# Optimization experiments

Measured on AMD Instinct MI355X. Metric: run time of the kernel, lower is better.

Reference implementation:

```python
import jax, jax.numpy as jnp
import numpy as np

ALPHA = 0.01
EPSB = ALPHA / (1.0 - 2.0 * ALPHA)  # boundary_eps
BIG = 1e9  # stands in for +inf; all real boundary distances are << box diameter


def setup_inputs() -> dict:
    key = jax.random.key(0)
    ks = jax.random.split(key, 8)
    B, D, K = 32768, 16, 1024
    return {
        "x": jax.random.normal(ks[0], (B, D), jnp.float32),
        "logp": jnp.zeros((B, 1), jnp.float32),
        "an1_w": 0.1 * jax.random.normal(ks[1], (D,), jnp.float32),
        "an1_b": 0.1 * jax.random.normal(ks[2], (D,), jnp.float32),
        "an2_w": 0.1 * jax.random.normal(ks[3], (D,), jnp.float32),
        "an2_b": 0.1 * jax.random.normal(ks[4], (D,), jnp.float32),
        "shift_coeff": jax.random.normal(ks[5], (D,), jnp.float32),
        "anchor_raw": jax.random.normal(ks[6], (1, K, D), jnp.float32),  # vorproj._anchor_pts
        "box_min": -4.0 * jnp.ones((D,), jnp.float32),
        "box_max": 4.0 * jnp.ones((D,), jnp.float32),
        "mixture_logits": jnp.zeros((K,), jnp.float32),
    }


def reference(x, logp, an1_w, an1_b, an2_w, an2_b, shift_coeff,
              anchor_raw, box_min, box_max, mixture_logits):
    B, D = x.shape
    # --- actnorm1: y = (x + b) * exp(w); logdet = sum(w) ---
    x = (x + an1_b) * jnp.exp(an1_w)
    logp = logp - jnp.sum(an1_w)
    # --- logit_transform.inverse: y = (sigmoid(x) - alpha) / (1 - 2*alpha) ---
    ld = jnp.sum(jax.nn.log_sigmoid(x) + jax.nn.log_sigmoid(-x), axis=1, keepdims=True) \
         - D * jnp.log(1.0 - 2.0 * ALPHA)
    x = (jax.nn.sigmoid(x) - ALPHA) / (1.0 - 2.0 * ALPHA)
    logp = logp - ld
    # --- (-eps, 1+eps) -> (0, 1) ---
    span = 1.0 + 2.0 * EPSB
    x = (x + EPSB) / span
    logp = logp + D * jnp.log(span)
    # --- scale into box constraints ---
    scale = box_max - box_min  # (D,)
    x = x * scale + box_min
    logp = logp - jnp.sum(jnp.log(scale))
    # --- anchor points: R -> (-1,1) -> (0,1) -> box ---
    a = anchor_raw[0]                       # (K, D)
    a = a / (1.0 + jnp.abs(a))
    a = (a + 1.0) * 0.5 * scale + box_min   # (K, D)
    K = a.shape[0]
    # --- find_nearest: argmin_k ||x - a_k||^2 (drop const ||x||^2) ---
    a_sq = jnp.sum(a * a, axis=1)                    # (K,)
    d2 = a_sq[None, :] - 2.0 * (x @ a.T)             # (B, K)
    k = jnp.argmin(d2, axis=1)                       # (B,)
    mask = jax.nn.one_hot(k, K, dtype=bool).reshape(B, 1, K)
    x_k = a[k]                                       # (B, D) gathered anchor
    # --- shift toward anchor: x + c*(x_k - x); logdet = sum log(1-c) ---
    c = jax.nn.sigmoid(shift_coeff) * 0.98 + 0.01
    x = x + c * (x_k - x)
    logp = logp - jnp.sum(jnp.log1p(-c))
    # --- map_outside_cell: radial map of Voronoi cell (within box) onto R^D ---
    dx = x - x_k
    r = jnp.sqrt(jnp.sum(dx * dx, axis=1))           # (B,)
    u = dx / jnp.maximum(r, 1e-12)[:, None]          # (B, D) unit direction
    # half-plane boundary distance t_j = (||a_j - a_k||^2 / 2) / (u . (a_j - a_k))
    proj = u @ a.T - jnp.sum(u * x_k, axis=1, keepdims=True)              # (B, K)
    halfdist = 0.5 * (a_sq[None, :] + a_sq[k][:, None] - 2.0 * (x_k @ a.T))  # (B, K)
    self_mask = jnp.arange(K)[None, :] == k[:, None]
    valid = jnp.logical_and(jnp.logical_not(self_mask), proj > 1e-12)
    t_half = jnp.where(valid, halfdist / jnp.where(valid, proj, 1.0), BIG)
    # box-face distances along u
    up = u > 1e-12
    un = u < -1e-12
    t_box = jnp.where(up, (box_max[None, :] - x_k) / jnp.where(up, u, 1.0),
            jnp.where(un, (box_min[None, :] - x_k) / jnp.where(un, u, 1.0), BIG))
    t = jnp.minimum(jnp.min(t_half, axis=1), jnp.min(t_box, axis=1))      # (B,)
    ratio = r / t                                     # in [0, 0.99] after shift
    s = 1.0 / (1.0 - ratio)
    x = x_k + dx * s[:, None]
    # logdet = (D+1) * log(t / (t - r)) = -(D+1) * log1p(-ratio)
    logp = logp + (D + 1.0) * jnp.log1p(-ratio)[:, None]
    # --- subtract cell center ---
    x = x - x_k
    # --- actnorm2 ---
    x = (x + an2_b) * jnp.exp(an2_w)
    logp = logp - jnp.sum(an2_w)
    # --- mixture component log-prob ---
    logprobs = jax.nn.log_softmax(mixture_logits)
    logp = logp - logprobs[k][:, None]
    return x, logp, mask
```

## Files before the change

kernel.cpp:

```cpp
#include <hip/hip_runtime.h>
#include <math.h>

#define DD 16
#define KK 1024

#define WS_A    0
#define WS_ASQ  16384
#define WS_OMC  17408
#define WS_B2   17424
#define WS_E2   17440
#define WS_MN   17456
#define WS_MX   17472
#define WS_SCL  17488
#define WS_DIM  17504
#define WS_E1   17520
#define WS_BASE 17536
#define WS_TOTD 17537
#define WS_NEED_BYTES (WS_TOTD * 8)

__device__ __forceinline__ double xformD(double rv, double mn, double scl) {
  double t = rv / (1.0 + fabs(rv));
  return (t + 1.0) * 0.5 * scl + mn;
}
__device__ __forceinline__ float xformF(float v, float mn, float mx) {
  return (v / (1.f + fabsf(v)) + 1.f) * 0.5f * (mx - mn) + mn;
}

__global__ __launch_bounds__(256) void vor_pre(
    const float* __restrict__ an1_w, const float* __restrict__ an2_w,
    const float* __restrict__ an2_b, const float* __restrict__ shift_c,
    const float* __restrict__ anchor_raw,
    const float* __restrict__ box_min, const float* __restrict__ box_max,
    const float* __restrict__ mlogits, double* __restrict__ ws)
{
  __shared__ double redD[16];
  const int tid = threadIdx.x;
  const int blk = blockIdx.x;

  if (blk == 0 && tid < DD) {
    double w1 = (double)an1_w[tid], w2 = (double)an2_w[tid];
    double sgc = 1.0 / (1.0 + exp(-(double)shift_c[tid]));
    double c = sgc * 0.98 + 0.01;
    double mn = (double)box_min[tid], mx = (double)box_max[tid];
    ws[WS_OMC + tid] = 1.0 - c;
    ws[WS_B2  + tid] = (double)an2_b[tid];
    ws[WS_E2  + tid] = exp(w2);
    ws[WS_MN  + tid] = mn;
    ws[WS_MX  + tid] = mx;
    ws[WS_SCL + tid] = mx - mn;
    ws[WS_E1  + tid] = exp(w1);
    ws[WS_DIM + tid] = -w1 - log(mx - mn) - log1p(-c) - w2;
  }
  const int j0 = blk * 64;
  for (int e = tid; e < 64 * DD; e += 256) {
    int j = j0 + (e >> 4), d = e & 15;
    double mn = (double)box_min[d];
    double scl = (double)box_max[d] - mn;
    ws[WS_A + (size_t)j * DD + d] = xformD((double)anchor_raw[j * DD + d], mn, scl);
  }
  __syncthreads();
  for (int j = j0 + tid; j < j0 + 64; j += 256) {
    double s = 0.0;
    #pragma unroll
    for (int d = 0; d < DD; ++d) { double a = ws[WS_A + (size_t)j * DD + d]; s = fma(a, a, s); }
    ws[WS_ASQ + j] = s;
  }
  if (blk != 0) return;
  float lm = -3.4e38f;
  for (int i = tid; i < KK; i += 256) lm = fmaxf(lm, mlogits[i]);
  #pragma unroll
  for (int o = 32; o > 0; o >>= 1) lm = fmaxf(lm, __shfl_xor(lm, o));
  if ((tid & 63) == 0) redD[tid >> 6] = (double)lm;
  __syncthreads();
  float gmax = (float)fmax(fmax(redD[0], redD[1]), fmax(redD[2], redD[3]));
  double lsum = 0.0;
  for (int i = tid; i < KK; i += 256) lsum += exp((double)mlogits[i] - (double)gmax);
  #pragma unroll
  for (int o = 32; o > 0; o >>= 1) lsum += __shfl_xor(lsum, o);
  if ((tid & 63) == 0) redD[4 + (tid >> 6)] = lsum;
  __syncthreads();
  if (tid == 0) {
    double lse = (double)gmax + log(redD[4] + redD[5] + redD[6] + redD[7]);
    double b = (double)DD * (log(0.98) + log(1.0 + 2.0 * (0.01 / 0.98)));
    #pragma unroll
    for (int d = 0; d < DD; ++d) b += ws[WS_DIM + d];
    ws[WS_BASE] = b + lse;
  }
}

#define NT2 1024
#define RPB2 128
#define SL2 8
#define JSL2 (KK / SL2)

__global__ __launch_bounds__(NT2, 4) void vor2(
    const float* __restrict__ x_in, const float* __restrict__ logp_in,
    const float* __restrict__ an1_b,
    const float* __restrict__ mlogits, const double* __restrict__ ws,
    float* __restrict__ out, int Brows)
{
  __shared__ __align__(16) float sA[KK][DD];
  __shared__ float sAsqH[KK];
  __shared__ float sX4T[DD][RPB2];
  __shared__ int   sPj[16][64];
  __shared__ float sRat[16][64];
  __shared__ int   sK[RPB2];
  __shared__ float sOmcF[DD], sB2F[DD], sE2F[DD], sMnF[DD], sMxF[DD];

  const int tid  = threadIdx.x;
  const int w    = tid >> 6;
  const int lane = tid & 63;
  const int rg   = w >> 3;
  const int sl   = w & 7;
  const int rrow = rg * 64 + lane;
  const int row  = blockIdx.x * RPB2 + rrow;
  const size_t coreEnd = (size_t)Brows * (DD + 1);

  if (tid < DD) {
    sOmcF[tid] = (float)ws[WS_OMC + tid];
    sB2F[tid]  = (float)ws[WS_B2 + tid];
    sE2F[tid]  = (float)ws[WS_E2 + tid];
    sMnF[tid]  = (float)ws[WS_MN + tid];
    sMxF[tid]  = (float)ws[WS_MX + tid];
  }
  for (int e = tid; e < KK * DD / 4; e += NT2) {
    double2 p0 = ((const double2*)(ws + WS_A))[e * 2 + 0];
    double2 p1 = ((const double2*)(ws + WS_A))[e * 2 + 1];
    ((float4*)sA)[e] = make_float4((float)p0.x, (float)p0.y, (float)p1.x, (float)p1.y);
  }
  __syncthreads();
  for (int j = tid; j < KK; j += NT2) {
    float acc = 0.f;
    #pragma unroll
    for (int d = 0; d < DD; ++d) { float a = sA[j][d]; acc = fmaf(a, a, acc); }
    sAsqH[j] = 0.5f * acc;
  }
  {
    float4* mz = (float4*)(out + coreEnd + (size_t)blockIdx.x * RPB2 * KK);
    #pragma unroll 4
    for (int i = tid; i < RPB2 * KK / 4; i += NT2)
      mz[i] = make_float4(0.f, 0.f, 0.f, 0.f);
  }

  const double A = 0.01, EPSB = 0.01 / 0.98;
  const double SPAN = 1.0 + 2.0 * EPSB;
  double lsigD = 0.0;
  if (sl == 0) {
    const float* xr = x_in + (size_t)row * DD;
    #pragma unroll
    for (int d = 0; d < DD; ++d) {
      double y1 = ((double)xr[d] + (double)an1_b[d]) * ws[WS_E1 + d];
      double sg = 1.0 / (1.0 + exp(-y1));
      double x2 = (sg - A) / (1.0 - 2.0 * A);
      double x3 = (x2 + EPSB) / SPAN;
      double x4 = x3 * ws[WS_SCL + d] + ws[WS_MN + d];
      sX4T[d][rrow] = (float)x4;
      double ay = fabs(y1);
      lsigD += ay + 2.0 * log1p(exp(-ay));
    }
  }
  __syncthreads();

  float x4f[DD];
  #pragma unroll
  for (int d = 0; d < DD; ++d) x4f[d] = sX4T[d][rrow];

  const int jlo = sl * JSL2, jhi = jlo + JSL2;
  float m1 = -3.4e38f, m2v = -3.4e38f;
  int j1 = jlo, j2v = jlo;
  #pragma unroll 2
  for (int j = jlo; j < jhi; ++j) {
    float acc = -sAsqH[j];
    const float4* ar = (const float4*)&sA[j][0];
    #pragma unroll
    for (int dq = 0; dq < 4; ++dq) {
      float4 a4 = ar[dq];
      acc = fmaf(x4f[4 * dq + 0], a4.x, acc);
      acc = fmaf(x4f[4 * dq + 1], a4.y, acc);
      acc = fmaf(x4f[4 * dq + 2], a4.z, acc);
      acc = fmaf(x4f[4 * dq + 3], a4.w, acc);
    }
    bool gt1 = acc > m1;
    bool gt2 = acc > m2v;
    m2v = gt1 ? m1 : (gt2 ? acc : m2v);
    j2v = gt1 ? j1 : (gt2 ? j : j2v);
    m1  = gt1 ? acc : m1;
    j1  = gt1 ? j : j1;
  }
  sPj[w][lane] = (j1 << 10) | j2v;
  __syncthreads();

  if (sl == 0) {
    double x4d[DD];
    {
      const float* xr = x_in + (size_t)row * DD;
      #pragma unroll
      for (int d = 0; d < DD; ++d) {
        double y1 = ((double)xr[d] + (double)an1_b[d]) * ws[WS_E1 + d];
        double sg = 1.0 / (1.0 + exp(-y1));
        double x2 = (sg - A) / (1.0 - 2.0 * A);
        double x3 = (x2 + EPSB) / SPAN;
        x4d[d] = x3 * ws[WS_SCL + d] + ws[WS_MN + d];
      }
    }
    double best = 1e300; int bk = 0x7fffffff;
    #pragma unroll
    for (int ss = 0; ss < SL2; ++ss) {
      int p = sPj[rg * 8 + ss][lane];
      #pragma unroll
      for (int t = 0; t < 2; ++t) {
        int j = t ? (p & 1023) : (p >> 10);
        const double* aj = ws + WS_A + (size_t)j * DD;
        double dot = 0.0;
        #pragma unroll
        for (int d = 0; d < DD; ++d) dot = fma(x4d[d], aj[d], dot);
        double d2 = ws[WS_ASQ + j] - 2.0 * dot;
        if (d2 < best || (d2 == best && j < bk)) { best = d2; bk = j; }
      }
    }
    sK[rrow] = bk;
  }
  __syncthreads();

  const int k = sK[rrow];

  float akf[DD], dxf[DD];
  float r2f = 0.f, dxak = 0.f;
  #pragma unroll
  for (int d = 0; d < DD; ++d) {
    float a = sA[k][d];
    akf[d] = a;
    float dx = sOmcF[d] * (x4f[d] - a);
    dxf[d] = dx;
    r2f  = fmaf(dx, dx, r2f);
    dxak = fmaf(dx, a, dxak);
  }
  const float rf   = sqrtf(r2f);
  const float rrf  = fmaxf(rf, 1e-12f);
  const float scal = rf / rrf;
  const float epsr = 1e-12f * rf;
  const float asqhk = sAsqH[k];

  float q1 = 0.f, h1 = 1.f;
  #pragma unroll 2
  for (int j = jlo; j < jhi; ++j) {
    float q = -dxak;
    float h = asqhk + sAsqH[j];
    const float4* ar = (const float4*)&sA[j][0];
    #pragma unroll
    for (int dq = 0; dq < 4; ++dq) {
      float4 a4 = ar[dq];
      q = fmaf(dxf[4 * dq + 0], a4.x, q);
      q = fmaf(dxf[4 * dq + 1], a4.y, q);
      q = fmaf(dxf[4 * dq + 2], a4.z, q);
      q = fmaf(dxf[4 * dq + 3], a4.w, q);
      h = fmaf(-akf[4 * dq + 0], a4.x, h);
      h = fmaf(-akf[4 * dq + 1], a4.y, h);
      h = fmaf(-akf[4 * dq + 2], a4.z, h);
      h = fmaf(-akf[4 * dq + 3], a4.w, h);
    }
    bool upd = (j != k) & (q > epsr) & (q * h1 > q1 * h);
    q1 = upd ? q : q1;
    h1 = upd ? h : h1;
  }
  sRat[w][lane] = scal * (q1 / h1);
  __syncthreads();

  if (sl == 0) {
    float ratio = rf * 1e-9f;
    #pragma unroll
    for (int ss = 0; ss < SL2; ++ss) ratio = fmaxf(ratio, sRat[rg * 8 + ss][lane]);
    #pragma unroll
    for (int d = 0; d < DD; ++d) {
      float uf = dxf[d] / rrf;
      if (uf > 1e-12f)        ratio = fmaxf(ratio, rf * uf / (sMxF[d] - akf[d]));
      else if (uf < -1e-12f)  ratio = fmaxf(ratio, rf * uf / (sMnF[d] - akf[d]));
    }
    float sS = 1.0f / (1.0f - ratio);
    float xo[DD];
    #pragma unroll
    for (int d = 0; d < DD; ++d)
      xo[d] = (dxf[d] * sS + sB2F[d]) * sE2F[d];
    float4* xp = (float4*)(out + (size_t)row * DD);
    xp[0] = make_float4(xo[0], xo[1], xo[2], xo[3]);
    xp[1] = make_float4(xo[4], xo[5], xo[6], xo[7]);
    xp[2] = make_float4(xo[8], xo[9], xo[10], xo[11]);
    xp[3] = make_float4(xo[12], xo[13], xo[14], xo[15]);
    double lp = (double)logp_in[row] + ws[WS_BASE] + lsigD
              + 17.0 * log1p(-(double)ratio)
              - (double)mlogits[k];
    out[(size_t)Brows * DD + row] = (float)lp;
    out[coreEnd + (size_t)row * KK + k] = 1.0f;
  }
}

#define NT 256
#define RPB 64
#define SLC4 4
#define JSL4 (KK / SLC4)

__global__ __launch_bounds__(NT, 2) void vor_green(
    const float* __restrict__ x_in, const float* __restrict__ logp_in,
    const float* __restrict__ an1_w, const float* __restrict__ an1_b,
    const float* __restrict__ an2_w, const float* __restrict__ an2_b,
    const float* __restrict__ shift_c, const float* __restrict__ anchor_raw,
    const float* __restrict__ box_min, const float* __restrict__ box_max,
    const float* __restrict__ mlogits,
    float* __restrict__ out, int Brows)
{
  __shared__ __align__(16) float sA[KK][DD];
  __shared__ float  sAsqH[KK];
  __shared__ float  sX4T[DD][RPB];
  __shared__ int    sPj1[SLC4][RPB], sPj2[SLC4][RPB];
  __shared__ int    sRI1[SLC4][RPB], sRI2[SLC4][RPB];
  __shared__ double sPartD[8];
  __shared__ double sE1D[DD], sB1D[DD], sOmcD[DD], sB2D[DD], sE2D[DD];
  __shared__ double sMnD[DD], sMxD[DD], sSclD[DD], sDimD[DD];
  __shared__ double sBaseD;
  __shared__ int    sKidx[RPB];

  const int tid  = threadIdx.x;
  const int sl   = tid >> 6;
  const int lane = tid & 63;
  const int row  = blockIdx.x * RPB + lane;
  const size_t coreEnd = (size_t)Brows * (DD + 1);

  for (int e = tid; e < KK * DD / 4; e += NT) {
    float4 raw = ((const float4*)anchor_raw)[e];
    float4 bmn = ((const float4*)box_min)[e & 3];
    float4 bmx = ((const float4*)box_max)[e & 3];
    float4 o;
    o.x = xformF(raw.x, bmn.x, bmx.x);
    o.y = xformF(raw.y, bmn.y, bmx.y);
    o.z = xformF(raw.z, bmn.z, bmx.z);
    o.w = xformF(raw.w, bmn.w, bmx.w);
    ((float4*)sA)[e] = o;
  }
  if (tid < DD) {
    double w1 = (double)an1_w[tid];
    sE1D[tid] = exp(w1);
    sB1D[tid] = (double)an1_b[tid];
    double sgc = 1.0 / (1.0 + exp(-(double)shift_c[tid]));
    double c = sgc * 0.98 + 0.01;
    sOmcD[tid] = 1.0 - c;
    double mn = (double)box_min[tid], mx = (double)box_max[tid];
    sMnD[tid] = mn; sMxD[tid] = mx; sSclD[tid] = mx - mn;
    double w2 = (double)an2_w[tid];
    sE2D[tid] = exp(w2);
    sB2D[tid] = (double)an2_b[tid];
    sDimD[tid] = -w1 - log(mx - mn) - log1p(-c) - w2;
  }
  __syncthreads();

  for (int j = tid; j < KK; j += NT) {
    float acc = 0.f;
    #pragma unroll
    for (int d = 0; d < DD; ++d) { float a = sA[j][d]; acc = fmaf(a, a, acc); }
    sAsqH[j] = 0.5f * acc;
  }

  float lm = -3.4e38f;
  for (int i = tid; i < KK; i += NT) lm = fmaxf(lm, mlogits[i]);
  #pragma unroll
  for (int o = 32; o > 0; o >>= 1) lm = fmaxf(lm, __shfl_xor(lm, o));
  if (lane == 0) sPartD[sl] = (double)lm;
  __syncthreads();
  float gmax = (float)fmax(fmax(sPartD[0], sPartD[1]), fmax(sPartD[2], sPartD[3]));
  double lsum = 0.0;
  for (int i = tid; i < KK; i += NT) lsum += exp((double)mlogits[i] - (double)gmax);
  #pragma unroll
  for (int o = 32; o > 0; o >>= 1) lsum += __shfl_xor(lsum, o);
  if (lane == 0) sPartD[4 + sl] = lsum;
  __syncthreads();
  if (tid == 0) {
    double lse = (double)gmax + log(sPartD[4] + sPartD[5] + sPartD[6] + sPartD[7]);
    double b = (double)DD * (log(0.98) + log(1.0 + 2.0 * (0.01 / 0.98)));
    #pragma unroll
    for (int d = 0; d < DD; ++d) b += sDimD[d];
    sBaseD = b + lse;
  }

  double x4d[DD];
  double lsigD = 0.0;
  if (sl == 0) {
    const double A = 0.01, EPSB = 0.01 / 0.98;
    const double SPAN = 1.0 + 2.0 * EPSB;
    const float* xr = x_in + (size_t)row * DD;
    #pragma unroll
    for (int d = 0; d < DD; ++d) {
      double y1 = ((double)xr[d] + sB1D[d]) * sE1D[d];
      double sg = 1.0 / (1.0 + exp(-y1));
      double x2 = (sg - A) / (1.0 - 2.0 * A);
      double x3 = (x2 + EPSB) / SPAN;
      double x4 = x3 * sSclD[d] + sMnD[d];
      x4d[d] = x4;
      sX4T[d][lane] = (float)x4;
      double ay = fabs(y1);
      lsigD += ay + 2.0 * log1p(exp(-ay));
    }
  }
  {
    float4* mz = (float4*)(out + coreEnd + (size_t)blockIdx.x * RPB * KK);
    #pragma unroll 4
    for (int i = tid; i < RPB * KK / 4; i += NT)
      mz[i] = make_float4(0.f, 0.f, 0.f, 0.f);
  }
  __syncthreads();

  float x4f[DD];
  #pragma unroll
  for (int d = 0; d < DD; ++d) x4f[d] = sX4T[d][lane];

  float m1 = -3.4e38f, m2v = -3.4e38f;
  int j1 = 0x7fffffff, j2v = 0x7fffffff;
  const int jlo = sl * JSL4, jhi = jlo + JSL4;
  #pragma unroll 2
  for (int j = jlo; j < jhi; ++j) {
    float acc = -sAsqH[j];
    const float4* ar = (const float4*)&sA[j][0];
    #pragma unroll
    for (int dq = 0; dq < 4; ++dq) {
      float4 a4 = ar[dq];
      acc = fmaf(x4f[4 * dq + 0], a4.x, acc);
      acc = fmaf(x4f[4 * dq + 1], a4.y, acc);
      acc = fmaf(x4f[4 * dq + 2], a4.z, acc);
      acc = fmaf(x4f[4 * dq + 3], a4.w, acc);
    }
    bool gt1 = acc > m1;
    bool gt2 = acc > m2v;
    m2v = gt1 ? m1 : (gt2 ? acc : m2v);
    j2v = gt1 ? j1 : (gt2 ? j : j2v);
    m1  = gt1 ? acc : m1;
    j1  = gt1 ? j : j1;
  }
  sPj1[sl][lane] = j1;
  sPj2[sl][lane] = j2v;
  __syncthreads();

  if (sl == 0) {
    double best = 1e300; int bk = 0x7fffffff;
    #pragma unroll
    for (int ss = 0; ss < SLC4; ++ss) {
      #pragma unroll
      for (int t = 0; t < 2; ++t) {
        int j = t ? sPj2[ss][lane] : sPj1[ss][lane];
        double asq = 0.0, dot = 0.0;
        #pragma unroll
        for (int d = 0; d < DD; ++d) {
          double a = xformD((double)anchor_raw[j * DD + d], sMnD[d], sSclD[d]);
          asq = fma(a, a, asq);
          dot = fma(x4d[d], a, dot);
        }
        double d2 = asq - 2.0 * dot;
        if (d2 < best || (d2 == best && j < bk)) { best = d2; bk = j; }
      }
    }
    sKidx[lane] = bk;
  }
  __syncthreads();

  const int k = sKidx[lane];

  float akf[DD], dxf[DD];
  float r2f = 0.f, dxak = 0.f;
  #pragma unroll
  for (int d = 0; d < DD; ++d) {
    float a = sA[k][d];
    akf[d] = a;
    float dx = (float)sOmcD[d] * (x4f[d] - a);
    dxf[d] = dx;
    r2f  = fmaf(dx, dx, r2f);
    dxak = fmaf(dx, a, dxak);
  }
  const float epsr = 1e-12f * sqrtf(r2f);
  const float asqhk = sAsqH[k];

  float q1 = 0.f, h1 = 1.f, q2 = 0.f, h2 = 1.f;
  int i1 = -1, i2 = -1;
  #pragma unroll 2
  for (int j = jlo; j < jhi; ++j) {
    float q = -dxak;
    float h = asqhk + sAsqH[j];
    const float4* ar = (const float4*)&sA[j][0];
    #pragma unroll
    for (int dq = 0; dq < 4; ++dq) {
      float4 a4 = ar[dq];
      q = fmaf(dxf[4 * dq + 0], a4.x, q);
      q = fmaf(dxf[4 * dq + 1], a4.y, q);
      q = fmaf(dxf[4 * dq + 2], a4.z, q);
      q = fmaf(dxf[4 * dq + 3], a4.w, q);
      h = fmaf(-akf[4 * dq + 0], a4.x, h);
      h = fmaf(-akf[4 * dq + 1], a4.y, h);
      h = fmaf(-akf[4 * dq + 2], a4.z, h);
      h = fmaf(-akf[4 * dq + 3], a4.w, h);
    }
    bool valid = (j != k) & (q > epsr);
    bool b1 = valid && (q * h1 > q1 * h);
    bool b2 = valid && (q * h2 > q2 * h);
    float nq2 = b1 ? q1 : (b2 ? q : q2);
    float nh2 = b1 ? h1 : (b2 ? h : h2);
    int   ni2 = b1 ? i1 : (b2 ? j : i2);
    q1 = b1 ? q : q1; h1 = b1 ? h : h1; i1 = b1 ? j : i1;
    q2 = nq2; h2 = nh2; i2 = ni2;
  }
  sRI1[sl][lane] = i1;
  sRI2[sl][lane] = i2;
  __syncthreads();

  if (sl == 0) {
    double akD[DD], dxD[DD];
    double r2 = 0.0;
    #pragma unroll
    for (int d = 0; d < DD; ++d) {
      double a = xformD((double)anchor_raw[k * DD + d], sMnD[d], sSclD[d]);
      akD[d] = a;
      double dx = sOmcD[d] * (x4d[d] - a);
      dxD[d] = dx;
      r2 = fma(dx, dx, r2);
    }
    double rD = sqrt(r2);
    double rr = fmax(rD, 1e-12);
    double ratio = rD / 1e9;

    #pragma unroll
    for (int ss = 0; ss < SLC4; ++ss) {
      #pragma unroll
      for (int t = 0; t < 2; ++t) {
        int j = t ? sRI2[ss][lane] : sRI1[ss][lane];
        if (j < 0 || j == k) continue;
        double q = 0.0, h = 0.0;
        #pragma unroll
        for (int d = 0; d < DD; ++d) {
          double aj = xformD((double)anchor_raw[j * DD + d], sMnD[d], sSclD[d]);
          double g = aj - akD[d];
          q = fma(dxD[d], g, q);
          h = fma(g, g, h);
        }
        double proj = q / rr;
        if (proj > 1e-12) {
          double cand = rD * proj / (0.5 * h);
          ratio = fmax(ratio, cand);
        }
      }
    }
    #pragma unroll
    for (int d = 0; d < DD; ++d) {
      double u = dxD[d] / rr;
      if (u > 1e-12)        ratio = fmax(ratio, rD * u / (sMxD[d] - akD[d]));
      else if (u < -1e-12)  ratio = fmax(ratio, rD * u / (sMnD[d] - akD[d]));
    }

    double sS = 1.0 / (1.0 - ratio);
    float* xo = out + (size_t)row * DD;
    #pragma unroll
    for (int d = 0; d < DD; ++d) {
      double x7 = dxD[d] * sS;
      double x8 = (x7 + sB2D[d]) * sE2D[d];
      xo[d] = (float)x8;
    }
    double lp = (double)logp_in[row] + sBaseD + lsigD
              + 17.0 * log1p(-ratio)
              - (double)mlogits[k];
    out[(size_t)Brows * DD + row] = (float)lp;
    out[coreEnd + (size_t)row * KK + k] = 1.0f;
  }
}

extern "C" void kernel_launch(void* const* d_in, const int* in_sizes, int n_in,
                              void* d_out, int out_size, void* d_ws, size_t ws_size,
                              hipStream_t stream) {
  (void)n_in; (void)out_size;
  const float* x_in   = (const float*)d_in[0];
  const float* logp   = (const float*)d_in[1];
  const float* an1w   = (const float*)d_in[2];
  const float* an1b   = (const float*)d_in[3];
  const float* an2w   = (const float*)d_in[4];
  const float* an2b   = (const float*)d_in[5];
  const float* shiftc = (const float*)d_in[6];
  const float* anchor = (const float*)d_in[7];
  const float* bmin   = (const float*)d_in[8];
  const float* bmax   = (const float*)d_in[9];
  const float* mlog   = (const float*)d_in[10];
  const int B = in_sizes[0] / DD;

  if (ws_size >= (size_t)WS_NEED_BYTES && d_ws != nullptr && (B % RPB2) == 0) {
    double* ws = (double*)d_ws;
    hipLaunchKernelGGL(vor_pre, dim3(16), dim3(256), 0, stream,
                       an1w, an2w, an2b, shiftc, anchor, bmin, bmax, mlog, ws);
    hipLaunchKernelGGL(vor2, dim3(B / RPB2), dim3(NT2), 0, stream,
                       x_in, logp, an1b, mlog,
                       (const double*)ws, (float*)d_out, B);
  } else {
    hipLaunchKernelGGL(vor_green, dim3(B / RPB), dim3(NT), 0, stream,
                       x_in, logp, an1w, an1b, an2w, an2b, shiftc, anchor,
                       bmin, bmax, mlog, (float*)d_out, B);
  }
}
```

Baseline: 109.3 us.

## Distribute double-precision nearest-anchor refinement across all slice waves

Result: no change. 111.1 us (+1.6%).

```diff
diff --git a/kernel.cpp b/kernel.cpp
--- a/kernel.cpp
+++ b/kernel.cpp
@@ -93,19 +93,18 @@
 #define SL2 8
 #define JSL2 (KK / SL2)
 
-__global__ __launch_bounds__(NT2, 4) void vor2(
+__global__ __launch_bounds__(NT2, 4) void vor3(
     const float* __restrict__ x_in, const float* __restrict__ logp_in,
     const float* __restrict__ an1_b,
     const float* __restrict__ mlogits, const double* __restrict__ ws,
     float* __restrict__ out, int Brows)
 {
   __shared__ __align__(16) float sA[KK][DD];
-  __shared__ float sAsqH[KK];
-  __shared__ float sX4T[DD][RPB2];
-  __shared__ int   sPj[16][64];
-  __shared__ float sRat[16][64];
-  __shared__ int   sK[RPB2];
-  __shared__ float sOmcF[DD], sB2F[DD], sE2F[DD], sMnF[DD], sMxF[DD];
+  __shared__ float  sAsqH[KK];
+  __shared__ double sD2[16][64];
+  __shared__ int    sJJ[16][64];
+  __shared__ float  sRat[16][64];
+  __shared__ float  sOmcF[DD], sB2F[DD], sE2F[DD], sMnF[DD], sMxF[DD];
 
   const int tid  = threadIdx.x;
   const int w    = tid >> 6;
@@ -144,8 +143,10 @@
 
   const double A = 0.01, EPSB = 0.01 / 0.98;
   const double SPAN = 1.0 + 2.0 * EPSB;
+  double x4d[DD];
+  float  x4f[DD];
   double lsigD = 0.0;
-  if (sl == 0) {
+  {
     const float* xr = x_in + (size_t)row * DD;
     #pragma unroll
     for (int d = 0; d < DD; ++d) {
@@ -154,16 +155,15 @@
       double x2 = (sg - A) / (1.0 - 2.0 * A);
       double x3 = (x2 + EPSB) / SPAN;
       double x4 = x3 * ws[WS_SCL + d] + ws[WS_MN + d];
-      sX4T[d][rrow] = (float)x4;
-      double ay = fabs(y1);
-      lsigD += ay + 2.0 * log1p(exp(-ay));
-    }
-  }
-  __syncthreads();
-
-  float x4f[DD];
-  #pragma unroll
-  for (int d = 0; d < DD; ++d) x4f[d] = sX4T[d][rrow];
+      x4d[d] = x4;
+      x4f[d] = (float)x4;
+      if (sl == 0) {
+        double ay = fabs(y1);
+        lsigD += ay + 2.0 * log1p(exp(-ay));
+      }
+    }
+  }
+  __syncthreads();
 
   const int jlo = sl * JSL2, jhi = jlo + JSL2;
   float m1 = -3.4e38f, m2v = -3.4e38f;
@@ -187,42 +187,34 @@
     m1  = gt1 ? acc : m1;
     j1  = gt1 ? j : j1;
   }
-  sPj[w][lane] = (j1 << 10) | j2v;
-  __syncthreads();
-
-  if (sl == 0) {
-    double x4d[DD];
-    {
-      const float* xr = x_in + (size_t)row * DD;
+
+  {
+    double bestD = 1e300; int bk = 0x7fffffff;
+    #pragma unroll
+    for (int t = 0; t < 2; ++t) {
+      int j = t ? j2v : j1;
+      const double* aj = ws + WS_A + (size_t)j * DD;
+      double dot = 0.0;
       #pragma unroll
-      for (int d = 0; d < DD; ++d) {
-        double y1 = ((double)xr[d] + (double)an1_b[d]) * ws[WS_E1 + d];
-        double sg = 1.0 / (1.0 + exp(-y1));
-        double x2 = (sg - A) / (1.0 - 2.0 * A);
-        double x3 = (x2 + EPSB) / SPAN;
-        x4d[d] = x3 * ws[WS_SCL + d] + ws[WS_MN + d];
-      }
-    }
-    double best = 1e300; int bk = 0x7fffffff;
+      for (int d = 0; d < DD; ++d) dot = fma(x4d[d], aj[d], dot);
+      double d2 = ws[WS_ASQ + j] - 2.0 * dot;
+      if (d2 < bestD || (d2 == bestD && j < bk)) { bestD = d2; bk = j; }
+    }
+    sD2[w][lane] = bestD;
+    sJJ[w][lane] = bk;
+  }
+  __syncthreads();
+
+  int k = 0x7fffffff;
+  {
+    double kb = 1e300;
     #pragma unroll
     for (int ss = 0; ss < SL2; ++ss) {
-      int p = sPj[rg * 8 + ss][lane];
-      #pragma unroll
-      for (int t = 0; t < 2; ++t) {
-        int j = t ? (p & 1023) : (p >> 10);
-        const double* aj = ws + WS_A + (size_t)j * DD;
-        double dot = 0.0;
-        #pragma unroll
-        for (int d = 0; d < DD; ++d) dot = fma(x4d[d], aj[d], dot);
-        double d2 = ws[WS_ASQ + j] - 2.0 * dot;
-        if (d2 < best || (d2 == best && j < bk)) { best = d2; bk = j; }
-      }
-    }
-    sK[rrow] = bk;
-  }
-  __syncthreads();
-
-  const int k = sK[rrow];
+      double d = sD2[rg * 8 + ss][lane];
+      int    j = sJJ[rg * 8 + ss][lane];
+      if (d < kb || (d == kb && j < k)) { kb = d; k = j; }
+    }
+  }
 
   float akf[DD], dxf[DD];
   float r2f = 0.f, dxak = 0.f;
@@ -587,7 +579,7 @@
     double* ws = (double*)d_ws;
     hipLaunchKernelGGL(vor_pre, dim3(16), dim3(256), 0, stream,
                        an1w, an2w, an2b, shiftc, anchor, bmin, bmax, mlog, ws);
-    hipLaunchKernelGGL(vor2, dim3(B / RPB2), dim3(NT2), 0, stream,
+    hipLaunchKernelGGL(vor3, dim3(B / RPB2), dim3(NT2), 0, stream,
                        x_in, logp, an1b, mlog,
                        (const double*)ws, (float*)d_out, B);
   } else {
```
